# Kernel tuning notes

Measured on AMD Instinct MI355X. Metric: run time of the kernel, lower is better.

The kernel has to match this reference:

```python
import jax, jax.numpy as jnp
import numpy as np
import math

B, S, D, H = 2, 2048, 1024, 16
DK = D // H


def setup_inputs() -> dict:
    key = jax.random.key(0)
    ks = jax.random.split(key, 8)
    scale = 1.0 / math.sqrt(D)
    inp = {
        "q": jax.random.normal(ks[0], (B, S, D), jnp.float32),
        "k": jax.random.normal(ks[1], (B, S, D), jnp.float32),
        "v": jax.random.normal(ks[2], (B, S, D), jnp.float32),
        # causal mask: 1 where attention allowed, 0 elsewhere
        "mask": jnp.tril(jnp.ones((S, S), jnp.int32))[None, None, :, :],
        "wq": jax.random.normal(ks[3], (D, D), jnp.float32) * scale,
        "bq": jnp.zeros((D,), jnp.float32),
        "wk": jax.random.normal(ks[4], (D, D), jnp.float32) * scale,
        "bk": jnp.zeros((D,), jnp.float32),
        "wv": jax.random.normal(ks[5], (D, D), jnp.float32) * scale,
        "bv": jnp.zeros((D,), jnp.float32),
        "wo": jax.random.normal(ks[6], (D, D), jnp.float32) * scale,
        "bo": jnp.zeros((D,), jnp.float32),
    }
    return inp


def _split_heads(x):
    # [B,S,D] -> [B,H,S,DK]
    b, s, _ = x.shape
    return x.reshape(b, s, H, DK).transpose(0, 2, 1, 3)


def reference(q, k, v, mask, wq, bq, wk, bk, wv, bv, wo, bo):
    # torch nn.Linear: y = x @ W.T + b
    qh = _split_heads(q @ wq.T + bq)   # [B,H,S,DK]
    kh = _split_heads(k @ wk.T + bk)
    vh = _split_heads(v @ wv.T + bv)
    scores = jnp.einsum("bhqd,bhkd->bhqk", qh, kh) / math.sqrt(DK)
    scores = jnp.where(mask == 0, jnp.float32(-1e9), scores)
    attn = jax.nn.softmax(scores, axis=-1)  # dropout p=0.0 -> identity
    ctx = jnp.einsum("bhqk,bhkd->bhqd", attn, vh)  # [B,H,S,DK]
    ctx = ctx.transpose(0, 2, 1, 3).reshape(q.shape[0], q.shape[1], D)
    return ctx @ wo.T + bo
```

## Files before the change

### kernel.cpp

```cpp
#include <hip/hip_runtime.h>
#include <hip/hip_bf16.h>

typedef __bf16 bf16;
typedef bf16  bf16x8 __attribute__((ext_vector_type(8)));
typedef bf16  bf16x4v __attribute__((ext_vector_type(4)));
typedef float f32x4 __attribute__((ext_vector_type(4)));

#define MFMA16(a, b, c) __builtin_amdgcn_mfma_f32_16x16x32_bf16(a, b, c, 0, 0, 0)

static constexpr int BB = 2, SS = 2048, DD = 1024, HH = 16, DKK = 64;

__device__ inline bf16x8 cvt8(const float* s) {
  const f32x4 a = *(const f32x4*)s;
  const f32x4 b = *(const f32x4*)(s + 4);
  bf16x8 r;
  r[0] = (bf16)a[0]; r[1] = (bf16)a[1]; r[2] = (bf16)a[2]; r[3] = (bf16)a[3];
  r[4] = (bf16)b[0]; r[5] = (bf16)b[1]; r[6] = (bf16)b[2]; r[7] = (bf16)b[3];
  return r;
}

__global__ __launch_bounds__(256) void cvt_qkv(
    const float* __restrict__ q, const float* __restrict__ k,
    const float* __restrict__ v,
    bf16* __restrict__ dq, bf16* __restrict__ dk, bf16* __restrict__ dv)
{
  const float* s = blockIdx.z == 0 ? q : blockIdx.z == 1 ? k : v;
  bf16*        d = blockIdx.z == 0 ? dq : blockIdx.z == 1 ? dk : dv;
  const size_t i = ((size_t)blockIdx.x * 256 + threadIdx.x) * 8;
  *(bf16x8*)(d + i) = cvt8(s + i);
}

__global__ __launch_bounds__(256) void cvt_w(
    const float* __restrict__ a, const float* __restrict__ b,
    const float* __restrict__ c, const float* __restrict__ d,
    bf16* __restrict__ da, bf16* __restrict__ db,
    bf16* __restrict__ dc, bf16* __restrict__ dd)
{
  const float* s = blockIdx.z == 0 ? a : blockIdx.z == 1 ? b
                 : blockIdx.z == 2 ? c : d;
  bf16*        o = blockIdx.z == 0 ? da : blockIdx.z == 1 ? db
                 : blockIdx.z == 2 ? dc : dd;
  const size_t i = ((size_t)blockIdx.x * 256 + threadIdx.x) * 8;
  *(bf16x8*)(o + i) = cvt8(s + i);
}

__device__ __forceinline__ void stage_load(bf16x8 (&r)[2], const bf16* __restrict__ g,
                                           int r0, int kb, int K, int tid) {
  #pragma unroll
  for (int j = 0; j < 2; ++j) {
    const int c   = tid + 256 * j;
    const int row = c >> 2;
    const int kg  = (c & 3) ^ (row & 3);
    r[j] = *(const bf16x8*)(g + (size_t)(r0 + row) * K + kb + kg * 8);
  }
}
__device__ __forceinline__ void stage_write(bf16* lds, const bf16x8 (&r)[2], int tid) {
  *(bf16x8*)(lds + (size_t)tid * 8)         = r[0];
  *(bf16x8*)(lds + (size_t)(tid + 256) * 8) = r[1];
}
__device__ __forceinline__ bf16x8 lds_frag(const bf16* buf, int row, int quad) {
  return *(const bf16x8*)(buf + (row * 4 + (quad ^ (row & 3))) * 8);
}

template <int OMODE>
__device__ __forceinline__ void gemm_core(
    const bf16* __restrict__ A, const bf16* __restrict__ W,
    const float* __restrict__ bias, void* __restrict__ Cp,
    bf16* As, bf16* Ws, int m0, int n0, int N, int K)
{
  const int tid  = threadIdx.x;
  const int wave = tid >> 6;
  const int lane = tid & 63;
  const int lm   = lane & 15;
  const int quad = lane >> 4;
  const int wm0  = (wave & 1) * 64;
  const int wn0  = (wave >> 1) * 64;

  f32x4 acc[4][4];
  #pragma unroll
  for (int mt = 0; mt < 4; ++mt)
    #pragma unroll
    for (int nt = 0; nt < 4; ++nt)
      acc[mt][nt] = {0.f, 0.f, 0.f, 0.f};

  bf16x8 ra[2], rw[2];
  stage_load(ra, A, m0, 0, K, tid);
  stage_load(rw, W, n0, 0, K, tid);
  stage_write(As, ra, tid);
  stage_write(Ws, rw, tid);
  __syncthreads();

  const int nk = K >> 5;
  for (int it = 0; it < nk; ++it) {
    const int cur = it & 1;
    if (it + 1 < nk) {
      stage_load(ra, A, m0, (it + 1) << 5, K, tid);
      stage_load(rw, W, n0, (it + 1) << 5, K, tid);
    }
    bf16x8 af[4], wf[4];
    #pragma unroll
    for (int mt = 0; mt < 4; ++mt) af[mt] = lds_frag(As + cur * 4096, wm0 + mt * 16 + lm, quad);
    #pragma unroll
    for (int nt = 0; nt < 4; ++nt) wf[nt] = lds_frag(Ws + cur * 4096, wn0 + nt * 16 + lm, quad);
    #pragma unroll
    for (int mt = 0; mt < 4; ++mt)
      #pragma unroll
      for (int nt = 0; nt < 4; ++nt)
        acc[mt][nt] = MFMA16(af[mt], wf[nt], acc[mt][nt]);
    if (it + 1 < nk) {
      stage_write(As + (cur ^ 1) * 4096, ra, tid);
      stage_write(Ws + (cur ^ 1) * 4096, rw, tid);
      __syncthreads();
    }
  }

  #pragma unroll
  for (int nt = 0; nt < 4; ++nt) {
    const int col = n0 + wn0 + nt * 16 + lm;
    const float bv = bias[col];
    #pragma unroll
    for (int mt = 0; mt < 4; ++mt) {
      const int row0 = m0 + wm0 + mt * 16 + quad * 4;
      if constexpr (OMODE == 1) {
        bf16* C = (bf16*)Cp;
        const int b = row0 >> 11, s = row0 & (SS - 1);
        bf16x4v vv;
        #pragma unroll
        for (int i = 0; i < 4; ++i) vv[i] = (bf16)(acc[mt][nt][i] + bv);
        *(bf16x4v*)(C + (size_t)b * DD * SS + (size_t)col * SS + s) = vv;
      } else if constexpr (OMODE == 0) {
        bf16* C = (bf16*)Cp;
        #pragma unroll
        for (int i = 0; i < 4; ++i)
          C[(size_t)(row0 + i) * N + col] = (bf16)(acc[mt][nt][i] + bv);
      } else {
        float* C = (float*)Cp;
        #pragma unroll
        for (int i = 0; i < 4; ++i)
          C[(size_t)(row0 + i) * N + col] = acc[mt][nt][i] + bv;
      }
    }
  }
}

__global__ __launch_bounds__(256, 3) void qkv_gemm(
    const bf16* __restrict__ qb, const bf16* __restrict__ kb2,
    const bf16* __restrict__ vb2,
    const bf16* __restrict__ wqb, const bf16* __restrict__ wkb,
    const bf16* __restrict__ wvb,
    const float* __restrict__ biq, const float* __restrict__ bik,
    const float* __restrict__ biv,
    bf16* __restrict__ Qp, bf16* __restrict__ Kp, bf16* __restrict__ Vpt)
{
  __shared__ __align__(16) bf16 As[2 * 4096];
  __shared__ __align__(16) bf16 Ws[2 * 4096];
  const int proj = blockIdx.x % 3;
  const int t    = blockIdx.x / 3;
  const int m0   = (t >> 3) << 7;
  const int n0   = (t & 7) << 7;
  if (proj == 0)      gemm_core<0>(qb,  wqb, biq, Qp,  As, Ws, m0, n0, DD, DD);
  else if (proj == 1) gemm_core<0>(kb2, wkb, bik, Kp,  As, Ws, m0, n0, DD, DD);
  else                gemm_core<1>(vb2, wvb, biv, Vpt, As, Ws, m0, n0, DD, DD);
}

__global__ __launch_bounds__(256, 3) void out_gemm(
    const bf16* __restrict__ Cx, const bf16* __restrict__ wob,
    const float* __restrict__ bo, float* __restrict__ out)
{
  __shared__ __align__(16) bf16 As[2 * 4096];
  __shared__ __align__(16) bf16 Ws[2 * 4096];
  const int m0 = (blockIdx.x >> 3) << 7;
  const int n0 = (blockIdx.x & 7) << 7;
  gemm_core<2>(Cx, wob, bo, out, As, Ws, m0, n0, DD, DD);
}

__global__ __launch_bounds__(256, 4) void flash_attn(
    const bf16* __restrict__ Qp, const bf16* __restrict__ Kp,
    const bf16* __restrict__ Vpt, bf16* __restrict__ Ctx)
{
  __shared__ __align__(16) bf16 Kt[2][64 * 64];
  __shared__ __align__(16) bf16 Vt[2][64 * 64];
  __shared__ __align__(16) bf16 Pt[4 * 16 * 64];

  const int tid  = threadIdx.x;
  const int wave = tid >> 6;
  const int lane = tid & 63;
  const int lm   = lane & 15;
  const int quad = lane >> 4;
  const int x7   = lm & 7;

  const int nchunk = SS / 64;
  const int bid = blockIdx.x;
  const int qc  = (nchunk - 1) - (bid % nchunk);
  const int h   = (bid / nchunk) % HH;
  const int b   = bid / (nchunk * HH);
  const int qb  = qc * 64;

  const int    headoff = h * DKK;
  const size_t base_bs = (size_t)b * SS;
  const size_t vbase   = (size_t)b * DD * SS + (size_t)headoff * SS;

  const float QSC = 0.18033688f;
  const int qrow = qb + wave * 16 + lm;
  const bf16* qptr = Qp + (base_bs + qrow) * DD + headoff + quad * 8;
  bf16x8 qa0 = *(const bf16x8*)(qptr);
  bf16x8 qa1 = *(const bf16x8*)(qptr + 32);
  #pragma unroll
  for (int j = 0; j < 8; ++j) {
    qa0[j] = (bf16)((float)qa0[j] * QSC);
    qa1[j] = (bf16)((float)qa1[j] * QSC);
  }

  const f32x4 vzero = {0.f, 0.f, 0.f, 0.f};
  f32x4 o[4];
  #pragma unroll
  for (int t = 0; t < 4; ++t) o[t] = vzero;
  float lrow[4] = {0.f, 0.f, 0.f, 0.f};
  int myrow[4];
  #pragma unroll
  for (int i = 0; i < 4; ++i) myrow[i] = qb + wave * 16 + quad * 4 + i;

  bf16* Pw = Pt + wave * 1024;
  const int ntiles = qb / 64 + 1;

  bf16x8 kr[2], vr[2];
  auto load_kv = [&](int t) {
    const int k0 = t * 64;
    #pragma unroll
    for (int j = 0; j < 2; ++j) {
      const int c  = tid + 256 * j;
      const int r  = c >> 3;
      const int gs = (c & 7) ^ (r & 7);
      kr[j] = *(const bf16x8*)(Kp + (base_bs + k0 + r) * DD + headoff + gs * 8);
      vr[j] = *(const bf16x8*)(Vpt + vbase + (size_t)r * SS + k0 + gs * 8);
    }
  };
  auto write_kv = [&](int buf) {
    #pragma unroll
    for (int j = 0; j < 2; ++j) {
      const int c = tid + 256 * j;
      *(bf16x8*)(Kt[buf] + c * 8) = kr[j];
      *(bf16x8*)(Vt[buf] + c * 8) = vr[j];
    }
  };

  load_kv(0);
  write_kv(0);
  __syncthreads();

  for (int t = 0; t < ntiles; ++t) {
    const int k0  = t * 64;
    const int cur = t & 1;
    if (t + 1 < ntiles) load_kv(t + 1);

    f32x4 s[4];
    #pragma unroll
    for (int kt = 0; kt < 4; ++kt) {
      const int key = kt * 16 + lm;
      const bf16x8 k0f = *(const bf16x8*)(Kt[cur] + key * 64 + ((quad)     ^ x7) * 8);
      const bf16x8 k1f = *(const bf16x8*)(Kt[cur] + key * 64 + ((4 + quad) ^ x7) * 8);
      s[kt] = MFMA16(qa1, k1f, MFMA16(qa0, k0f, vzero));
    }

    const bool edge = (t == ntiles - 1);
    #pragma unroll
    for (int kt = 0; kt < 4; ++kt) {
      const int key = k0 + kt * 16 + lm;
      const int kg  = 2 * kt + (lm >> 3);
      #pragma unroll
      for (int i = 0; i < 4; ++i) {
        float p = __builtin_amdgcn_exp2f(s[kt][i]);
        if (edge && key > myrow[i]) p = 0.f;
        lrow[i] += p;
        const int r = quad * 4 + i;
        Pw[r * 64 + (kg ^ (r & 7)) * 8 + x7] = (bf16)p;
      }
    }

    const bf16x8 pa0 = *(const bf16x8*)(Pw + lm * 64 + ((quad)     ^ x7) * 8);
    const bf16x8 pa1 = *(const bf16x8*)(Pw + lm * 64 + ((4 + quad) ^ x7) * 8);
    #pragma unroll
    for (int tt = 0; tt < 4; ++tt) {
      const int d = tt * 16 + lm;
      const bf16x8 v0f = *(const bf16x8*)(Vt[cur] + d * 64 + ((quad)     ^ x7) * 8);
      const bf16x8 v1f = *(const bf16x8*)(Vt[cur] + d * 64 + ((4 + quad) ^ x7) * 8);
      o[tt] = MFMA16(pa1, v1f, MFMA16(pa0, v0f, o[tt]));
    }

    if (t + 1 < ntiles) {
      write_kv(cur ^ 1);
      __syncthreads();
    }
  }

  #pragma unroll
  for (int off = 1; off < 16; off <<= 1)
    #pragma unroll
    for (int i = 0; i < 4; ++i) lrow[i] += __shfl_xor(lrow[i], off, 64);

  #pragma unroll
  for (int i = 0; i < 4; ++i) {
    const float inv = (lrow[i] > 0.f) ? 1.0f / lrow[i] : 0.f;
    const int row = myrow[i];
    #pragma unroll
    for (int tt = 0; tt < 4; ++tt)
      Ctx[(base_bs + row) * DD + headoff + tt * 16 + lm] = (bf16)(o[tt][i] * inv);
  }
}

extern "C" void kernel_launch(void* const* d_in, const int* in_sizes, int n_in,
                              void* d_out, int out_size, void* d_ws, size_t ws_size,
                              hipStream_t stream)
{
  const float* q  = (const float*)d_in[0];
  const float* k  = (const float*)d_in[1];
  const float* v  = (const float*)d_in[2];
  const float* wq = (const float*)d_in[4];
  const float* bq = (const float*)d_in[5];
  const float* wk = (const float*)d_in[6];
  const float* bk = (const float*)d_in[7];
  const float* wv = (const float*)d_in[8];
  const float* bv = (const float*)d_in[9];
  const float* wo = (const float*)d_in[10];
  const float* bo = (const float*)d_in[11];
  float* out = (float*)d_out;

  const size_t MK = (size_t)BB * SS * DD;
  const size_t WK = (size_t)DD * DD;

  bf16* qb  = (bf16*)d_ws;
  bf16* kb2 = qb  + MK;
  bf16* vb2 = kb2 + MK;
  bf16* Qp  = vb2 + MK;
  bf16* Kp  = Qp  + MK;
  bf16* Vpt = Kp  + MK;
  bf16* wqb = Vpt + MK;
  bf16* wkb = wqb + WK;
  bf16* wvb = wkb + WK;
  bf16* wob = wvb + WK;
  bf16* Cx  = qb;

  dim3 blk(256);

  cvt_qkv<<<dim3(2048, 1, 3), blk, 0, stream>>>(q, k, v, qb, kb2, vb2);
  cvt_w<<<dim3(512, 1, 4), blk, 0, stream>>>(wq, wk, wv, wo, wqb, wkb, wvb, wob);

  qkv_gemm<<<dim3(768), blk, 0, stream>>>(qb, kb2, vb2, wqb, wkb, wvb,
                                          bq, bk, bv, Qp, Kp, Vpt);
  flash_attn<<<dim3(BB * HH * (SS / 64)), blk, 0, stream>>>(Qp, Kp, Vpt, Cx);
  out_gemm<<<dim3(256), blk, 0, stream>>>(Cx, wob, bo, out);
}
```

Baseline: 250.7 us.

## Use async global-to-LDS loads, pair causal chunks, merge conversion kernels

GEMM and attention tiles are now staged with global_load_lds direct-to-LDS loads instead of going through registers. Flash attention pairs a long and a short causal query chunk per block, halving the grid and balancing work. Occupancy drops to 2 blocks per CU. GEMM tile order changes to walk M fastest, and the two fp32-to-bf16 conversion kernels are merged into one launch. There is a risk that the async loads are not waited on before the barrier, since no explicit vmcnt wait is inserted.

```diff
diff --git a/kernel.cpp b/kernel.cpp
--- a/kernel.cpp
+++ b/kernel.cpp
@@ -10,7 +10,13 @@
 
 static constexpr int BB = 2, SS = 2048, DD = 1024, HH = 16, DKK = 64;
 
-__device__ inline bf16x8 cvt8(const float* s) {
+__device__ __forceinline__ void async16(const void* g, void* l) {
+  __builtin_amdgcn_global_load_lds(
+      (const __attribute__((address_space(1))) void*)g,
+      (__attribute__((address_space(3))) void*)l, 16, 0, 0);
+}
+
+__device__ __forceinline__ bf16x8 cvt8(const float* s) {
   const f32x4 a = *(const f32x4*)s;
   const f32x4 b = *(const f32x4*)(s + 4);
   bf16x8 r;
@@ -19,44 +25,41 @@
   return r;
 }
 
-__global__ __launch_bounds__(256) void cvt_qkv(
+__global__ __launch_bounds__(256) void cvt_all(
     const float* __restrict__ q, const float* __restrict__ k,
     const float* __restrict__ v,
-    bf16* __restrict__ dq, bf16* __restrict__ dk, bf16* __restrict__ dv)
-{
-  const float* s = blockIdx.z == 0 ? q : blockIdx.z == 1 ? k : v;
-  bf16*        d = blockIdx.z == 0 ? dq : blockIdx.z == 1 ? dk : dv;
+    const float* __restrict__ wq, const float* __restrict__ wk,
+    const float* __restrict__ wv, const float* __restrict__ wo,
+    bf16* __restrict__ dq, bf16* __restrict__ dk, bf16* __restrict__ dv,
+    bf16* __restrict__ dwq, bf16* __restrict__ dwk,
+    bf16* __restrict__ dwv, bf16* __restrict__ dwo)
+{
   const size_t i = ((size_t)blockIdx.x * 256 + threadIdx.x) * 8;
-  *(bf16x8*)(d + i) = cvt8(s + i);
-}
-
-__global__ __launch_bounds__(256) void cvt_w(
-    const float* __restrict__ a, const float* __restrict__ b,
-    const float* __restrict__ c, const float* __restrict__ d,
-    bf16* __restrict__ da, bf16* __restrict__ db,
-    bf16* __restrict__ dc, bf16* __restrict__ dd)
-{
-  const float* s = blockIdx.z == 0 ? a : blockIdx.z == 1 ? b
-                 : blockIdx.z == 2 ? c : d;
-  bf16*        o = blockIdx.z == 0 ? da : blockIdx.z == 1 ? db
-                 : blockIdx.z == 2 ? dc : dd;
-  const size_t i = ((size_t)blockIdx.x * 256 + threadIdx.x) * 8;
-  *(bf16x8*)(o + i) = cvt8(s + i);
-}
-
-__device__ __forceinline__ void stage_load(bf16x8 (&r)[2], const bf16* __restrict__ g,
-                                           int r0, int kb, int K, int tid) {
+  const int z = blockIdx.z;
+  const float* s;
+  bf16* d;
+  size_t off = i;
+  if (z == 0)      { s = q; d = dq; }
+  else if (z == 1) { s = k; d = dk; }
+  else if (z == 2) { s = v; d = dv; }
+  else {
+    const int seg = (int)(i >> 20);
+    off = i & ((1u << 20) - 1);
+    s = seg == 0 ? wq : seg == 1 ? wk : seg == 2 ? wv : wo;
+    d = seg == 0 ? dwq : seg == 1 ? dwk : seg == 2 ? dwv : dwo;
+  }
+  *(bf16x8*)(d + off) = cvt8(s + off);
+}
+
+__device__ __forceinline__ void stage_async(bf16* lds, const bf16* __restrict__ g,
+                                            int r0, int kb, int K, int tid) {
   #pragma unroll
   for (int j = 0; j < 2; ++j) {
     const int c   = tid + 256 * j;
     const int row = c >> 2;
     const int kg  = (c & 3) ^ (row & 3);
-    r[j] = *(const bf16x8*)(g + (size_t)(r0 + row) * K + kb + kg * 8);
-  }
-}
-__device__ __forceinline__ void stage_write(bf16* lds, const bf16x8 (&r)[2], int tid) {
-  *(bf16x8*)(lds + (size_t)tid * 8)         = r[0];
-  *(bf16x8*)(lds + (size_t)(tid + 256) * 8) = r[1];
+    async16(g + (size_t)(r0 + row) * K + kb + kg * 8, lds + (size_t)c * 8);
+  }
 }
 __device__ __forceinline__ bf16x8 lds_frag(const bf16* buf, int row, int quad) {
   return *(const bf16x8*)(buf + (row * 4 + (quad ^ (row & 3))) * 8);
@@ -83,19 +86,16 @@
     for (int nt = 0; nt < 4; ++nt)
       acc[mt][nt] = {0.f, 0.f, 0.f, 0.f};
 
-  bf16x8 ra[2], rw[2];
-  stage_load(ra, A, m0, 0, K, tid);
-  stage_load(rw, W, n0, 0, K, tid);
-  stage_write(As, ra, tid);
-  stage_write(Ws, rw, tid);
+  stage_async(As, A, m0, 0, K, tid);
+  stage_async(Ws, W, n0, 0, K, tid);
   __syncthreads();
 
   const int nk = K >> 5;
   for (int it = 0; it < nk; ++it) {
     const int cur = it & 1;
     if (it + 1 < nk) {
-      stage_load(ra, A, m0, (it + 1) << 5, K, tid);
-      stage_load(rw, W, n0, (it + 1) << 5, K, tid);
+      stage_async(As + (cur ^ 1) * 4096, A, m0, (it + 1) << 5, K, tid);
+      stage_async(Ws + (cur ^ 1) * 4096, W, n0, (it + 1) << 5, K, tid);
     }
     bf16x8 af[4], wf[4];
     #pragma unroll
@@ -107,11 +107,7 @@
       #pragma unroll
       for (int nt = 0; nt < 4; ++nt)
         acc[mt][nt] = MFMA16(af[mt], wf[nt], acc[mt][nt]);
-    if (it + 1 < nk) {
-      stage_write(As + (cur ^ 1) * 4096, ra, tid);
-      stage_write(Ws + (cur ^ 1) * 4096, rw, tid);
-      __syncthreads();
-    }
+    if (it + 1 < nk) __syncthreads();
   }
 
   #pragma unroll
@@ -154,10 +150,10 @@
 {
   __shared__ __align__(16) bf16 As[2 * 4096];
   __shared__ __align__(16) bf16 Ws[2 * 4096];
-  const int proj = blockIdx.x % 3;
-  const int t    = blockIdx.x / 3;
-  const int m0   = (t >> 3) << 7;
-  const int n0   = (t & 7) << 7;
+  const int proj = blockIdx.x >> 8;
+  const int r    = blockIdx.x & 255;
+  const int n0   = (r >> 5) << 7;
+  const int m0   = (r & 31) << 7;
   if (proj == 0)      gemm_core<0>(qb,  wqb, biq, Qp,  As, Ws, m0, n0, DD, DD);
   else if (proj == 1) gemm_core<0>(kb2, wkb, bik, Kp,  As, Ws, m0, n0, DD, DD);
   else                gemm_core<1>(vb2, wvb, biv, Vpt, As, Ws, m0, n0, DD, DD);
@@ -169,12 +165,12 @@
 {
   __shared__ __align__(16) bf16 As[2 * 4096];
   __shared__ __align__(16) bf16 Ws[2 * 4096];
-  const int m0 = (blockIdx.x >> 3) << 7;
-  const int n0 = (blockIdx.x & 7) << 7;
+  const int n0 = (blockIdx.x >> 5) << 7;
+  const int m0 = (blockIdx.x & 31) << 7;
   gemm_core<2>(Cx, wob, bo, out, As, Ws, m0, n0, DD, DD);
 }
 
-__global__ __launch_bounds__(256, 4) void flash_attn(
+__global__ __launch_bounds__(256, 2) void flash_attn(
     const bf16* __restrict__ Qp, const bf16* __restrict__ Kp,
     const bf16* __restrict__ Vpt, bf16* __restrict__ Ctx)
 {
@@ -189,122 +185,115 @@
   const int quad = lane >> 4;
   const int x7   = lm & 7;
 
-  const int nchunk = SS / 64;
-  const int bid = blockIdx.x;
-  const int qc  = (nchunk - 1) - (bid % nchunk);
-  const int h   = (bid / nchunk) % HH;
-  const int b   = bid / (nchunk * HH);
-  const int qb  = qc * 64;
+  const int jp = blockIdx.x & 15;
+  const int bh = blockIdx.x >> 4;
+  const int h  = bh & (HH - 1);
+  const int b  = bh >> 4;
 
   const int    headoff = h * DKK;
   const size_t base_bs = (size_t)b * SS;
   const size_t vbase   = (size_t)b * DD * SS + (size_t)headoff * SS;
 
   const float QSC = 0.18033688f;
-  const int qrow = qb + wave * 16 + lm;
-  const bf16* qptr = Qp + (base_bs + qrow) * DD + headoff + quad * 8;
-  bf16x8 qa0 = *(const bf16x8*)(qptr);
-  bf16x8 qa1 = *(const bf16x8*)(qptr + 32);
-  #pragma unroll
-  for (int j = 0; j < 8; ++j) {
-    qa0[j] = (bf16)((float)qa0[j] * QSC);
-    qa1[j] = (bf16)((float)qa1[j] * QSC);
-  }
-
   const f32x4 vzero = {0.f, 0.f, 0.f, 0.f};
-  f32x4 o[4];
-  #pragma unroll
-  for (int t = 0; t < 4; ++t) o[t] = vzero;
-  float lrow[4] = {0.f, 0.f, 0.f, 0.f};
-  int myrow[4];
-  #pragma unroll
-  for (int i = 0; i < 4; ++i) myrow[i] = qb + wave * 16 + quad * 4 + i;
-
   bf16* Pw = Pt + wave * 1024;
-  const int ntiles = qb / 64 + 1;
-
-  bf16x8 kr[2], vr[2];
-  auto load_kv = [&](int t) {
-    const int k0 = t * 64;
-    #pragma unroll
-    for (int j = 0; j < 2; ++j) {
-      const int c  = tid + 256 * j;
-      const int r  = c >> 3;
-      const int gs = (c & 7) ^ (r & 7);
-      kr[j] = *(const bf16x8*)(Kp + (base_bs + k0 + r) * DD + headoff + gs * 8);
-      vr[j] = *(const bf16x8*)(Vpt + vbase + (size_t)r * SS + k0 + gs * 8);
-    }
-  };
-  auto write_kv = [&](int buf) {
-    #pragma unroll
-    for (int j = 0; j < 2; ++j) {
-      const int c = tid + 256 * j;
-      *(bf16x8*)(Kt[buf] + c * 8) = kr[j];
-      *(bf16x8*)(Vt[buf] + c * 8) = vr[j];
-    }
-  };
-
-  load_kv(0);
-  write_kv(0);
-  __syncthreads();
-
-  for (int t = 0; t < ntiles; ++t) {
-    const int k0  = t * 64;
-    const int cur = t & 1;
-    if (t + 1 < ntiles) load_kv(t + 1);
-
-    f32x4 s[4];
-    #pragma unroll
-    for (int kt = 0; kt < 4; ++kt) {
-      const int key = kt * 16 + lm;
-      const bf16x8 k0f = *(const bf16x8*)(Kt[cur] + key * 64 + ((quad)     ^ x7) * 8);
-      const bf16x8 k1f = *(const bf16x8*)(Kt[cur] + key * 64 + ((4 + quad) ^ x7) * 8);
-      s[kt] = MFMA16(qa1, k1f, MFMA16(qa0, k0f, vzero));
-    }
-
-    const bool edge = (t == ntiles - 1);
-    #pragma unroll
-    for (int kt = 0; kt < 4; ++kt) {
-      const int key = k0 + kt * 16 + lm;
-      const int kg  = 2 * kt + (lm >> 3);
-      #pragma unroll
-      for (int i = 0; i < 4; ++i) {
-        float p = __builtin_amdgcn_exp2f(s[kt][i]);
-        if (edge && key > myrow[i]) p = 0.f;
-        lrow[i] += p;
-        const int r = quad * 4 + i;
-        Pw[r * 64 + (kg ^ (r & 7)) * 8 + x7] = (bf16)p;
-      }
-    }
-
-    const bf16x8 pa0 = *(const bf16x8*)(Pw + lm * 64 + ((quad)     ^ x7) * 8);
-    const bf16x8 pa1 = *(const bf16x8*)(Pw + lm * 64 + ((4 + quad) ^ x7) * 8);
-    #pragma unroll
-    for (int tt = 0; tt < 4; ++tt) {
-      const int d = tt * 16 + lm;
-      const bf16x8 v0f = *(const bf16x8*)(Vt[cur] + d * 64 + ((quad)     ^ x7) * 8);
-      const bf16x8 v1f = *(const bf16x8*)(Vt[cur] + d * 64 + ((4 + quad) ^ x7) * 8);
-      o[tt] = MFMA16(pa1, v1f, MFMA16(pa0, v0f, o[tt]));
-    }
-
-    if (t + 1 < ntiles) {
-      write_kv(cur ^ 1);
+
+  #pragma unroll 1
+  for (int pass = 0; pass < 2; ++pass) {
+    const int qc = pass == 0 ? (31 - jp) : jp;
+    const int qb = qc * 64;
+
+    const int qrow = qb + wave * 16 + lm;
+    const bf16* qptr = Qp + (base_bs + qrow) * DD + headoff + quad * 8;
+    bf16x8 qa0 = *(const bf16x8*)(qptr);
+    bf16x8 qa1 = *(const bf16x8*)(qptr + 32);
+    #pragma unroll
+    for (int jj = 0; jj < 8; ++jj) {
+      qa0[jj] = (bf16)((float)qa0[jj] * QSC);
+      qa1[jj] = (bf16)((float)qa1[jj] * QSC);
+    }
+
+    f32x4 o[4];
+    #pragma unroll
+    for (int t = 0; t < 4; ++t) o[t] = vzero;
+    float lrow[4] = {0.f, 0.f, 0.f, 0.f};
+    int myrow[4];
+    #pragma unroll
+    for (int i = 0; i < 4; ++i) myrow[i] = qb + wave * 16 + quad * 4 + i;
+
+    auto stage_kv = [&](int buf, int t) {
+      const int k0 = t * 64;
+      #pragma unroll
+      for (int j = 0; j < 2; ++j) {
+        const int c  = tid + 256 * j;
+        const int r  = c >> 3;
+        const int gs = (c & 7) ^ (r & 7);
+        async16(Kp + (base_bs + k0 + r) * DD + headoff + gs * 8,
+                Kt[buf] + (size_t)c * 8);
+        async16(Vpt + vbase + (size_t)r * SS + k0 + gs * 8,
+                Vt[buf] + (size_t)c * 8);
+      }
+    };
+
+    const int ntiles = qc + 1;
+    stage_kv(0, 0);
+    __syncthreads();
+
+    for (int t = 0; t < ntiles; ++t) {
+      const int k0  = t * 64;
+      const int cur = t & 1;
+      if (t + 1 < ntiles) stage_kv(cur ^ 1, t + 1);
+
+      f32x4 s[4];
+      #pragma unroll
+      for (int kt = 0; kt < 4; ++kt) {
+        const int key = kt * 16 + lm;
+        const bf16x8 k0f = *(const bf16x8*)(Kt[cur] + key * 64 + ((quad)     ^ x7) * 8);
+        const bf16x8 k1f = *(const bf16x8*)(Kt[cur] + key * 64 + ((4 + quad) ^ x7) * 8);
+        s[kt] = MFMA16(qa1, k1f, MFMA16(qa0, k0f, vzero));
+      }
+
+      const bool edge = (t == ntiles - 1);
+      #pragma unroll
+      for (int kt = 0; kt < 4; ++kt) {
+        const int key = k0 + kt * 16 + lm;
+        const int kg  = 2 * kt + (lm >> 3);
+        #pragma unroll
+        for (int i = 0; i < 4; ++i) {
+          float p = __builtin_amdgcn_exp2f(s[kt][i]);
+          if (edge && key > myrow[i]) p = 0.f;
+          lrow[i] += p;
+          const int r = quad * 4 + i;
+          Pw[r * 64 + (kg ^ (r & 7)) * 8 + x7] = (bf16)p;
+        }
+      }
+
+      const bf16x8 pa0 = *(const bf16x8*)(Pw + lm * 64 + ((quad)     ^ x7) * 8);
+      const bf16x8 pa1 = *(const bf16x8*)(Pw + lm * 64 + ((4 + quad) ^ x7) * 8);
+      #pragma unroll
+      for (int tt = 0; tt < 4; ++tt) {
+        const int d = tt * 16 + lm;
+        const bf16x8 v0f = *(const bf16x8*)(Vt[cur] + d * 64 + ((quad)     ^ x7) * 8);
+        const bf16x8 v1f = *(const bf16x8*)(Vt[cur] + d * 64 + ((4 + quad) ^ x7) * 8);
+        o[tt] = MFMA16(pa1, v1f, MFMA16(pa0, v0f, o[tt]));
+      }
+
       __syncthreads();
     }
-  }
-
-  #pragma unroll
-  for (int off = 1; off < 16; off <<= 1)
-    #pragma unroll
-    for (int i = 0; i < 4; ++i) lrow[i] += __shfl_xor(lrow[i], off, 64);
-
-  #pragma unroll
-  for (int i = 0; i < 4; ++i) {
-    const float inv = (lrow[i] > 0.f) ? 1.0f / lrow[i] : 0.f;
-    const int row = myrow[i];
-    #pragma unroll
-    for (int tt = 0; tt < 4; ++tt)
-      Ctx[(base_bs + row) * DD + headoff + tt * 16 + lm] = (bf16)(o[tt][i] * inv);
+
+    #pragma unroll
+    for (int off = 1; off < 16; off <<= 1)
+      #pragma unroll
+      for (int i = 0; i < 4; ++i) lrow[i] += __shfl_xor(lrow[i], off, 64);
+
+    #pragma unroll
+    for (int i = 0; i < 4; ++i) {
+      const float inv = (lrow[i] > 0.f) ? 1.0f / lrow[i] : 0.f;
+      const int row = myrow[i];
+      #pragma unroll
+      for (int tt = 0; tt < 4; ++tt)
+        Ctx[(base_bs + row) * DD + headoff + tt * 16 + lm] = (bf16)(o[tt][i] * inv);
+    }
   }
 }
 
@@ -342,11 +331,10 @@
 
   dim3 blk(256);
 
-  cvt_qkv<<<dim3(2048, 1, 3), blk, 0, stream>>>(q, k, v, qb, kb2, vb2);
-  cvt_w<<<dim3(512, 1, 4), blk, 0, stream>>>(wq, wk, wv, wo, wqb, wkb, wvb, wob);
-
+  cvt_all<<<dim3(2048, 1, 4), blk, 0, stream>>>(q, k, v, wq, wk, wv, wo,
+                                                qb, kb2, vb2, wqb, wkb, wvb, wob);
   qkv_gemm<<<dim3(768), blk, 0, stream>>>(qb, kb2, vb2, wqb, wkb, wvb,
                                           bq, bk, bv, Qp, Kp, Vpt);
-  flash_attn<<<dim3(BB * HH * (SS / 64)), blk, 0, stream>>>(Qp, Kp, Vpt, Cx);
+  flash_attn<<<dim3(BB * HH * 16), blk, 0, stream>>>(Qp, Kp, Vpt, Cx);
   out_gemm<<<dim3(256), blk, 0, stream>>>(Cx, wob, bo, out);
 }
```

New measurement: 235.7 us. -6.0%, faster.
